# Kernel tuning notes

Measured on AMD Instinct MI355X. Metric: run time of the kernel, lower is better.

The kernel has to match this reference:

```python
import jax, jax.numpy as jnp
import numpy as np
from jax import lax

N, GH, GE, LH, LL = 19, 64, 64, 64, 2
B, T = 256, 256


def _normalized_adjacency(A):
    # A: (..., n, n). Add self-loops, symmetric degree normalization.
    n = A.shape[-1]
    A = A + jnp.eye(n, dtype=A.dtype)
    deg = jnp.clip(A.sum(axis=-1), 1e-6, None)  # (..., n)
    dis = deg ** -0.5
    return A * dis[..., :, None] * dis[..., None, :]


def _graph_encoder(A, w1_w, w1_b, w2_w, w2_b):
    # A: (B, T, n, n) -> (B, T, GE). Node features X = A rows.
    An = _normalized_adjacency(A)
    X = jax.nn.relu(An @ (A @ w1_w.T + w1_b))   # (B,T,n,GH)
    X = jax.nn.relu(An @ (X @ w2_w.T + w2_b))   # (B,T,n,GE)
    return X.mean(axis=-2)


def _lstm_layer(x, Wih, Whh, bih, bhh):
    # x: (B, T, D); PyTorch gate order i,f,g,o. Returns (B, T, H).
    Bb = x.shape[0]
    H = Whh.shape[1]
    xg = x @ Wih.T + (bih + bhh)  # precompute input contributions (B,T,4H)

    def step(carry, xt):
        h, c = carry
        gates = xt + h @ Whh.T
        i, f, g, o = jnp.split(gates, 4, axis=-1)
        c = jax.nn.sigmoid(f) * c + jax.nn.sigmoid(i) * jnp.tanh(g)
        h = jax.nn.sigmoid(o) * jnp.tanh(c)
        return (h, c), h

    h0 = jnp.zeros((Bb, H), x.dtype)
    (_, _), hs = lax.scan(step, (h0, h0), jnp.swapaxes(xg, 0, 1))
    return jnp.swapaxes(hs, 0, 1)


def setup_inputs() -> dict:
    key = jax.random.key(0)
    ks = jax.random.split(key, 20)
    s = 0.1
    inp = {
        'conn': jax.random.uniform(ks[0], (B, T, N, N), jnp.float32),
        'mask': jnp.ones((B, T), jnp.int32),
        'w1_w': jax.random.normal(ks[1], (GH, N), jnp.float32) * s,
        'w1_b': jax.random.normal(ks[2], (GH,), jnp.float32) * s,
        'w2_w': jax.random.normal(ks[3], (GE, GH), jnp.float32) * s,
        'w2_b': jax.random.normal(ks[4], (GE,), jnp.float32) * s,
        'lstm_Wih0': jax.random.normal(ks[5], (4 * LH, GE), jnp.float32) * s,
        'lstm_Whh0': jax.random.normal(ks[6], (4 * LH, LH), jnp.float32) * s,
        'lstm_bih0': jax.random.normal(ks[7], (4 * LH,), jnp.float32) * s,
        'lstm_bhh0': jax.random.normal(ks[8], (4 * LH,), jnp.float32) * s,
        'lstm_Wih1': jax.random.normal(ks[9], (4 * LH, LH), jnp.float32) * s,
        'lstm_Whh1': jax.random.normal(ks[10], (4 * LH, LH), jnp.float32) * s,
        'lstm_bih1': jax.random.normal(ks[11], (4 * LH,), jnp.float32) * s,
        'lstm_bhh1': jax.random.normal(ks[12], (4 * LH,), jnp.float32) * s,
        'fc1_w': jax.random.normal(ks[13], (32, LH), jnp.float32) * s,
        'fc1_b': jax.random.normal(ks[14], (32,), jnp.float32) * s,
        'fc2_w': jax.random.normal(ks[15], (2, 32), jnp.float32) * s,
        'fc2_b': jax.random.normal(ks[16], (2,), jnp.float32) * s,
    }
    return inp


def reference(conn, mask, w1_w, w1_b, w2_w, w2_b,
              lstm_Wih0, lstm_Whh0, lstm_bih0, lstm_bhh0,
              lstm_Wih1, lstm_Whh1, lstm_bih1, lstm_bhh1,
              fc1_w, fc1_b, fc2_w, fc2_b):
    emb = _graph_encoder(conn, w1_w, w1_b, w2_w, w2_b)  # (B,T,GE)
    mf = mask.astype(emb.dtype)
    emb = emb * mf[:, :, None]
    out = _lstm_layer(emb, lstm_Wih0, lstm_Whh0, lstm_bih0, lstm_bhh0)
    out = _lstm_layer(out, lstm_Wih1, lstm_Whh1, lstm_bih1, lstm_bhh1)  # (B,T,LH)
    lengths = jnp.clip(mask.sum(axis=1), 1, None)
    last_idx = jnp.clip(lengths - 1, 0, None)  # (B,)
    last_h = jnp.take_along_axis(out, last_idx[:, None, None], axis=1)[:, 0, :]
    h = jax.nn.relu(last_h @ fc1_w.T + fc1_b)
    return h @ fc2_w.T + fc2_b  # (B,2) logits
```

## Files before the change

### kernel.cpp

```cpp
#include <hip/hip_runtime.h>
#include <hip/hip_bf16.h>
#include <math.h>

#define GN 19
#define BB 256
#define TT 256

typedef short short8 __attribute__((ext_vector_type(8)));
typedef float f4 __attribute__((ext_vector_type(4)));

union Frag { int i[4]; short8 s; };

#define LWAIT() __asm__ volatile("s_waitcnt lgkmcnt(0)" ::: "memory")
#define WGBAR() __asm__ volatile("s_waitcnt lgkmcnt(0)\ns_barrier" ::: "memory")
#define PIN8(x) __asm__ volatile("" : "+v"(x))
#define PINF(x) __asm__ volatile("" : "+v"(x))

#define MFMA(a,b,c) __builtin_amdgcn_mfma_f32_16x16x32_bf16(a,b,c,0,0,0)

__device__ __forceinline__ int pkbf(float a, float b) {
    __hip_bfloat162 h2 = __float22bfloat162_rn(make_float2(a, b));
    union { __hip_bfloat162 h; int i; } u; u.h = h2; return u.i;
}

__device__ __forceinline__ float fexp2(float x) { return __builtin_amdgcn_exp2f(x); }
__device__ __forceinline__ float frcp(float x)  { return __builtin_amdgcn_rcpf(x); }
__device__ __forceinline__ float sigm(float x)  { return frcp(1.f + fexp2(-1.4426950408889634f * x)); }
__device__ __forceinline__ float tanha(float x) { float e = fexp2(2.8853900817779268f * x); return 1.f - 2.f * frcp(e + 1.f); }

__global__ __launch_bounds__(64) void encoder_mfma(
    const float* __restrict__ conn,
    const int*   __restrict__ mask,
    const float* __restrict__ w1_w,
    const float* __restrict__ w1_b,
    const float* __restrict__ w2_w,
    const float* __restrict__ w2_b,
    float* __restrict__ emb,
    int num_graphs)
{
    __shared__ float S[2304];
    __shared__ float dis[32];
    __shared__ float ps[256];

    const int t = threadIdx.x;
    const int l15 = t & 15;
    const int quad = t >> 4;

    float km[8];
    #pragma unroll
    for (int j = 0; j < 8; ++j) km[j] = (quad * 8 + j < GN) ? 1.f : 0.f;

    int rr[6], cc[6];
    #pragma unroll
    for (int i = 0; i < 6; ++i) {
        int e = t + 64 * i;
        rr[i] = e / GN;
        cc[i] = e - rr[i] * GN;
    }

    Frag w1F[4];
    #pragma unroll
    for (int nt = 0; nt < 4; ++nt) {
        int n = nt * 16 + l15;
        #pragma unroll
        for (int p = 0; p < 4; ++p) {
            int k0 = quad * 8 + 2 * p, k1 = k0 + 1;
            float a = (k0 < GN) ? w1_w[n * GN + k0] : 0.f;
            float b = (k1 < GN) ? w1_w[n * GN + k1] : 0.f;
            w1F[nt].i[p] = pkbf(a, b);
        }
    }
    Frag w2F[2][4];
    #pragma unroll
    for (int kt = 0; kt < 2; ++kt)
        #pragma unroll
        for (int nt = 0; nt < 4; ++nt) {
            int n = nt * 16 + l15;
            #pragma unroll
            for (int p = 0; p < 4; ++p) {
                int k = kt * 32 + quad * 8 + 2 * p;
                w2F[kt][nt].i[p] = pkbf(w2_w[n * 64 + k], w2_w[n * 64 + k + 1]);
            }
        }
    float b1v[4], b2v[4];
    #pragma unroll
    for (int nt = 0; nt < 4; ++nt) {
        b1v[nt] = w1_b[nt * 16 + l15];
        b2v[nt] = w2_b[nt * 16 + l15];
    }

    float pf[6];
    {
        int g0 = blockIdx.x < num_graphs ? blockIdx.x : 0;
        const float* Ag = conn + (size_t)g0 * (GN * GN);
        #pragma unroll
        for (int i = 0; i < 6; ++i) {
            int e = t + 64 * i;
            if (e < GN * GN) pf[i] = Ag[e];
        }
    }

    #pragma unroll 1
    for (int g = blockIdx.x; g < num_graphs; g += gridDim.x) {
        #pragma unroll
        for (int i = 0; i < 4; ++i) {
            int s = t + 64 * i;
            int row = s >> 3, c4 = s & 7;
            f4 z = {0.f, 0.f, 0.f, 0.f};
            *(f4*)&S[row * 68 + c4 * 4] = z;
        }
        LWAIT();
        #pragma unroll
        for (int i = 0; i < 6; ++i) {
            if (t + 64 * i < GN * GN) S[rr[i] * 68 + cc[i]] = pf[i];
        }
        {
            int gn = g + gridDim.x;
            const float* Ag = conn + (size_t)(gn < num_graphs ? gn : g) * (GN * GN);
            #pragma unroll
            for (int i = 0; i < 6; ++i) {
                int e = t + 64 * i;
                if (e < GN * GN) pf[i] = Ag[e];
            }
        }
        LWAIT();

        if (t < 32) {
            float dv = 0.f;
            if (t < GN) {
                float d = 1.0f;
                #pragma unroll
                for (int c4 = 0; c4 < 8; ++c4) {
                    f4 v = *(f4*)&S[t * 68 + c4 * 4];
                    d += v.x + v.y + v.z + v.w;
                }
                dv = rsqrtf(d);
            }
            dis[t] = dv;
        }
        LWAIT();

        float dk[8];
        {
            f4 v0 = *(f4*)&dis[quad * 8];
            f4 v1 = *(f4*)&dis[quad * 8 + 4];
            dk[0]=v0.x; dk[1]=v0.y; dk[2]=v0.z; dk[3]=v0.w;
            dk[4]=v1.x; dk[5]=v1.y; dk[6]=v1.z; dk[7]=v1.w;
        }
        Frag aF[2], anF[2];
        #pragma unroll
        for (int mt = 0; mt < 2; ++mt) {
            int m = l15 + 16 * mt;
            float dm = dis[m];
            f4 v0 = *(f4*)&S[m * 68 + quad * 8];
            f4 v1 = *(f4*)&S[m * 68 + quad * 8 + 4];
            float av[8] = {v0.x, v0.y, v0.z, v0.w, v1.x, v1.y, v1.z, v1.w};
            float an[8];
            #pragma unroll
            for (int j = 0; j < 8; ++j) {
                int k = quad * 8 + j;
                an[j] = (av[j] + (m == k ? 1.f : 0.f)) * dm * dk[j];
            }
            #pragma unroll
            for (int p = 0; p < 4; ++p) {
                aF[mt].i[p]  = pkbf(av[2*p], av[2*p+1]);
                anF[mt].i[p] = pkbf(an[2*p], an[2*p+1]);
            }
        }
        LWAIT();

        #pragma unroll
        for (int mt = 0; mt < 2; ++mt)
            #pragma unroll
            for (int nt = 0; nt < 4; ++nt) {
                float bb = b1v[nt];
                f4 c = {bb, bb, bb, bb};
                c = MFMA(aF[mt].s, w1F[nt].s, c);
                int col = nt * 16 + l15;
                #pragma unroll
                for (int r = 0; r < 4; ++r)
                    S[col * 36 + (mt * 16 + quad * 4 + r)] = c[r];
            }
        LWAIT();

        Frag hF[4];
        #pragma unroll
        for (int nt = 0; nt < 4; ++nt) {
            int n = nt * 16 + l15;
            f4 v0 = *(f4*)&S[n * 36 + quad * 8];
            f4 v1 = *(f4*)&S[n * 36 + quad * 8 + 4];
            float vv[8] = {v0.x, v0.y, v0.z, v0.w, v1.x, v1.y, v1.z, v1.w};
            #pragma unroll
            for (int p = 0; p < 4; ++p)
                hF[nt].i[p] = pkbf(vv[2*p] * km[2*p], vv[2*p+1] * km[2*p+1]);
        }
        LWAIT();

        #pragma unroll
        for (int mt = 0; mt < 2; ++mt)
            #pragma unroll
            for (int nt = 0; nt < 4; ++nt) {
                f4 c = {0.f, 0.f, 0.f, 0.f};
                c = MFMA(anF[mt].s, hF[nt].s, c);
                int col = nt * 16 + l15;
                #pragma unroll
                for (int r = 0; r < 4; ++r)
                    S[(mt * 16 + quad * 4 + r) * 68 + col] = fmaxf(c[r], 0.f);
            }
        LWAIT();

        Frag xF[2][2];
        #pragma unroll
        for (int mt = 0; mt < 2; ++mt) {
            int m = l15 + 16 * mt;
            #pragma unroll
            for (int kt = 0; kt < 2; ++kt) {
                f4 v0 = *(f4*)&S[m * 68 + kt * 32 + quad * 8];
                f4 v1 = *(f4*)&S[m * 68 + kt * 32 + quad * 8 + 4];
                xF[mt][kt].i[0] = pkbf(v0.x, v0.y);
                xF[mt][kt].i[1] = pkbf(v0.z, v0.w);
                xF[mt][kt].i[2] = pkbf(v1.x, v1.y);
                xF[mt][kt].i[3] = pkbf(v1.z, v1.w);
            }
        }
        LWAIT();

        #pragma unroll
        for (int mt = 0; mt < 2; ++mt)
            #pragma unroll
            for (int nt = 0; nt < 4; ++nt) {
                float bb = b2v[nt];
                f4 c = {bb, bb, bb, bb};
                c = MFMA(xF[mt][0].s, w2F[0][nt].s, c);
                c = MFMA(xF[mt][1].s, w2F[1][nt].s, c);
                int col = nt * 16 + l15;
                #pragma unroll
                for (int r = 0; r < 4; ++r)
                    S[col * 36 + (mt * 16 + quad * 4 + r)] = c[r];
            }
        LWAIT();

        Frag hG[4];
        #pragma unroll
        for (int nt = 0; nt < 4; ++nt) {
            int n = nt * 16 + l15;
            f4 v0 = *(f4*)&S[n * 36 + quad * 8];
            f4 v1 = *(f4*)&S[n * 36 + quad * 8 + 4];
            float vv[8] = {v0.x, v0.y, v0.z, v0.w, v1.x, v1.y, v1.z, v1.w};
            #pragma unroll
            for (int p = 0; p < 4; ++p)
                hG[nt].i[p] = pkbf(vv[2*p] * km[2*p], vv[2*p+1] * km[2*p+1]);
        }

        float cs[4];
        #pragma unroll
        for (int nt = 0; nt < 4; ++nt) cs[nt] = 0.f;
        #pragma unroll
        for (int mt = 0; mt < 2; ++mt)
            #pragma unroll
            for (int nt = 0; nt < 4; ++nt) {
                f4 c = {0.f, 0.f, 0.f, 0.f};
                c = MFMA(anF[mt].s, hG[nt].s, c);
                if (mt == 0) {
                    cs[nt] += fmaxf(c[0], 0.f) + fmaxf(c[1], 0.f)
                            + fmaxf(c[2], 0.f) + fmaxf(c[3], 0.f);
                } else if (quad == 0) {
                    cs[nt] += fmaxf(c[0], 0.f) + fmaxf(c[1], 0.f) + fmaxf(c[2], 0.f);
                }
            }
        #pragma unroll
        for (int nt = 0; nt < 4; ++nt)
            ps[quad * 64 + nt * 16 + l15] = cs[nt];
        LWAIT();
        float tot = ps[t] + ps[64 + t] + ps[128 + t] + ps[192 + t];
        float mf = (float)mask[g];
        emb[(size_t)g * 64 + t] = tot * (1.f / 19.f) * mf;
        LWAIT();
    }
}

__device__ __forceinline__ void unpack_h(const int* __restrict__ src,
                                         int l15, int quad,
                                         Frag* __restrict__ BHh,
                                         Frag* __restrict__ BHl)
{
    #pragma unroll
    for (int kt = 0; kt < 2; ++kt) {
        const int4* pp = (const int4*)&src[l15 * 68 + kt * 32 + quad * 8];
        int4 va = pp[0], vb = pp[1];
        BHh[kt].i[0] = (int)__builtin_amdgcn_perm((unsigned)va.y, (unsigned)va.x, 0x05040100u);
        BHh[kt].i[1] = (int)__builtin_amdgcn_perm((unsigned)va.w, (unsigned)va.z, 0x05040100u);
        BHh[kt].i[2] = (int)__builtin_amdgcn_perm((unsigned)vb.y, (unsigned)vb.x, 0x05040100u);
        BHh[kt].i[3] = (int)__builtin_amdgcn_perm((unsigned)vb.w, (unsigned)vb.z, 0x05040100u);
        BHl[kt].i[0] = (int)__builtin_amdgcn_perm((unsigned)va.y, (unsigned)va.x, 0x07060302u);
        BHl[kt].i[1] = (int)__builtin_amdgcn_perm((unsigned)va.w, (unsigned)va.z, 0x07060302u);
        BHl[kt].i[2] = (int)__builtin_amdgcn_perm((unsigned)vb.y, (unsigned)vb.x, 0x07060302u);
        BHl[kt].i[3] = (int)__builtin_amdgcn_perm((unsigned)vb.w, (unsigned)vb.z, 0x07060302u);
    }
}

__global__ __launch_bounds__(1024, 4) void lstm_mfma(
    const float* __restrict__ x,
    const int*   __restrict__ mask,
    const float* __restrict__ Wih0, const float* __restrict__ Whh0,
    const float* __restrict__ bih0, const float* __restrict__ bhh0,
    const float* __restrict__ Wih1, const float* __restrict__ Whh1,
    const float* __restrict__ bih1, const float* __restrict__ bhh1,
    const float* __restrict__ fc1_w, const float* __restrict__ fc1_b,
    const float* __restrict__ fc2_w, const float* __restrict__ fc2_b,
    float* __restrict__ out)
{
    __shared__ int   h0b[2][16 * 68];
    __shared__ int   h1b[2][16 * 68];
    __shared__ float hlast[16][68];
    __shared__ float red[512];
    __shared__ int   li_s[16];

    const int tid  = threadIdx.x;
    const int w    = tid >> 6;
    const int grp  = w >> 3;
    const int wl   = w & 7;
    const int lane = tid & 63;
    const int l15  = lane & 15;
    const int quad = lane >> 4;
    const int bb0  = blockIdx.x * 16;

    for (int i = tid; i < 16 * 68; i += 1024) h1b[0][i] = 0;

    if (tid < 512) {
        int b16 = tid >> 5, j = tid & 31;
        int s = 0;
        #pragma unroll
        for (int c8 = 0; c8 < 8; ++c8)
            s += mask[(bb0 + b16) * TT + j + 32 * c8];
        red[tid] = (float)s;
    }
    __syncthreads();
    if (tid < 16) {
        float s = 0.f;
        #pragma unroll
        for (int j = 0; j < 32; ++j) s += red[tid * 32 + j];
        int li = (int)s - 1;
        li_s[tid] = li < 0 ? 0 : (li > TT - 1 ? TT - 1 : li);
    }
    __syncthreads();
    const int li = li_s[l15];

    const float* __restrict__ Wx = grp ? Wih1 : Wih0;
    const float* __restrict__ Wh = grp ? Whh1 : Whh0;
    const float* __restrict__ bi = grp ? bih1 : bih0;
    const float* __restrict__ bh = grp ? bhh1 : bhh0;

    Frag Ax[2][2], Ah[2][2];
    f4 biasv[2];
    #pragma unroll
    for (int mt = 0; mt < 2; ++mt) {
        int mg = 2 * wl + mt;
        int orig = (l15 & 3) * 64 + (mg * 4 + (l15 >> 2));
        #pragma unroll
        for (int kt = 0; kt < 2; ++kt)
            #pragma unroll
            for (int p = 0; p < 4; ++p) {
                int k = kt * 32 + quad * 8 + 2 * p;
                Ax[mt][kt].i[p] = pkbf(Wx[orig * 64 + k], Wx[orig * 64 + k + 1]);
                Ah[mt][kt].i[p] = pkbf(Wh[orig * 64 + k], Wh[orig * 64 + k + 1]);
            }
        int uu = mg * 4 + quad;
        #pragma unroll
        for (int r = 0; r < 4; ++r)
            biasv[mt][r] = bi[r * 64 + uu] + bh[r * 64 + uu];
    }
    #pragma unroll
    for (int mt = 0; mt < 2; ++mt) {
        PIN8(Ax[mt][0].s); PIN8(Ax[mt][1].s);
        PIN8(Ah[mt][0].s); PIN8(Ah[mt][1].s);
        PINF(biasv[mt]);
    }

    const int u0 = (2 * wl + 0) * 4 + quad;
    const int u1 = (2 * wl + 1) * 4 + quad;

    Frag BX[2], BH0h[2], BH0l[2], BH1h[2], BH1l[2];
    #pragma unroll
    for (int kt = 0; kt < 2; ++kt)
        #pragma unroll
        for (int p = 0; p < 4; ++p) {
            BX[kt].i[p] = 0; BH0h[kt].i[p] = 0; BH0l[kt].i[p] = 0;
            BH1h[kt].i[p] = 0; BH1l[kt].i[p] = 0;
        }
    float cst[2] = {0.f, 0.f}, hlv[2] = {0.f, 0.f};

    const float* __restrict__ xb = x + (size_t)(bb0 + l15) * TT * 64;
    f4 xpre[4];
    if (grp == 0) {
        const f4* p0 = (const f4*)(xb + quad * 8);
        const f4* p1 = (const f4*)(xb + 32 + quad * 8);
        xpre[0] = p0[0]; xpre[1] = p0[1];
        xpre[2] = p1[0]; xpre[3] = p1[1];
    }

    #pragma unroll 1
    for (int it = 0; it <= TT; ++it) {
        const int cur = it & 1;
        f4 g[2];
        bool act = false;

        if (grp == 0) {
            if (it < TT) {
                act = true;
                #pragma unroll
                for (int kt = 0; kt < 2; ++kt) {
                    f4 v0 = xpre[kt * 2], v1 = xpre[kt * 2 + 1];
                    BX[kt].i[0] = pkbf(v0.x, v0.y);
                    BX[kt].i[1] = pkbf(v0.z, v0.w);
                    BX[kt].i[2] = pkbf(v1.x, v1.y);
                    BX[kt].i[3] = pkbf(v1.z, v1.w);
                }
                int tn = it + 1 < TT ? it + 1 : TT - 1;
                const f4* p0 = (const f4*)(xb + (size_t)tn * 64 + quad * 8);
                const f4* p1 = (const f4*)(xb + (size_t)tn * 64 + 32 + quad * 8);
                xpre[0] = p0[0]; xpre[1] = p0[1];
                xpre[2] = p1[0]; xpre[3] = p1[1];

                #pragma unroll
                for (int mt = 0; mt < 2; ++mt) {
                    f4 ca = biasv[mt];
                    ca = MFMA(Ax[mt][0].s, BX[0].s,   ca);
                    ca = MFMA(Ah[mt][0].s, BH0h[0].s, ca);
                    ca = MFMA(Ah[mt][0].s, BH0l[0].s, ca);
                    f4 cb = {0.f, 0.f, 0.f, 0.f};
                    cb = MFMA(Ax[mt][1].s, BX[1].s,   cb);
                    cb = MFMA(Ah[mt][1].s, BH0h[1].s, cb);
                    cb = MFMA(Ah[mt][1].s, BH0l[1].s, cb);
                    g[mt] = ca + cb;
                }
            }
        } else {
            if (it >= 1) {
                act = true;
                #pragma unroll
                for (int mt = 0; mt < 2; ++mt) {
                    f4 ca = biasv[mt];
                    ca = MFMA(Ax[mt][0].s, BH0h[0].s, ca);
                    ca = MFMA(Ax[mt][0].s, BH0l[0].s, ca);
                    ca = MFMA(Ah[mt][0].s, BH1h[0].s, ca);
                    ca = MFMA(Ah[mt][0].s, BH1l[0].s, ca);
                    f4 cb = {0.f, 0.f, 0.f, 0.f};
                    cb = MFMA(Ax[mt][1].s, BH0h[1].s, cb);
                    cb = MFMA(Ax[mt][1].s, BH0l[1].s, cb);
                    cb = MFMA(Ah[mt][1].s, BH1h[1].s, cb);
                    cb = MFMA(Ah[mt][1].s, BH1l[1].s, cb);
                    g[mt] = ca + cb;
                }
            }
        }

        if (act) {
            int* __restrict__ dst = grp ? h1b[cur] : h0b[cur];
            #pragma unroll
            for (int mt = 0; mt < 2; ++mt) {
                f4 gg = g[mt];
                float si = sigm(gg[0]), sf = sigm(gg[1]);
                float tg = tanha(gg[2]), so = sigm(gg[3]);
                float cc = fmaf(sf, cst[mt], si * tg);
                cst[mt] = cc;
                float h = so * tanha(cc);
                if (grp && it - 1 == li) hlv[mt] = h;
                unsigned hb = __float_as_uint(h);
                float hhi = __uint_as_float(hb & 0xFFFF0000u);
                float hlo = h - hhi;
                unsigned lopk = (unsigned)pkbf(hlo, hlo);
                int packed = (int)__builtin_amdgcn_perm(lopk, hb, 0x05040302u);
                dst[l15 * 68 + (mt ? u1 : u0)] = packed;
            }
        }

        WGBAR();

        if (it < TT) {
            unpack_h(h0b[cur], l15, quad, BH0h, BH0l);
            if (grp) unpack_h(h1b[cur], l15, quad, BH1h, BH1l);
        }
    }

    if (grp == 1) {
        hlast[l15][u0] = hlv[0];
        hlast[l15][u1] = hlv[1];
    }
    __syncthreads();
    if (tid < 512) {
        int b = tid >> 5, o = tid & 31;
        float acc = fc1_b[o];
        const float* fw = fc1_w + o * 64;
        #pragma unroll
        for (int j = 0; j < 64; ++j)
            acc = fmaf(hlast[b][j], fw[j], acc);
        red[b * 32 + o] = fmaxf(acc, 0.f);
    }
    __syncthreads();
    if (tid < 32) {
        int b = tid >> 1, o = tid & 1;
        float acc = fc2_b[o];
        #pragma unroll
        for (int j = 0; j < 32; ++j)
            acc = fmaf(fc2_w[o * 32 + j], red[b * 32 + j], acc);
        out[(bb0 + b) * 2 + o] = acc;
    }
}

extern "C" void kernel_launch(void* const* d_in, const int* in_sizes, int n_in,
                              void* d_out, int out_size, void* d_ws, size_t ws_size,
                              hipStream_t stream)
{
    const float* conn  = (const float*)d_in[0];
    const int*   mask  = (const int*)  d_in[1];
    const float* w1_w  = (const float*)d_in[2];
    const float* w1_b  = (const float*)d_in[3];
    const float* w2_w  = (const float*)d_in[4];
    const float* w2_b  = (const float*)d_in[5];
    const float* Wih0  = (const float*)d_in[6];
    const float* Whh0  = (const float*)d_in[7];
    const float* bih0  = (const float*)d_in[8];
    const float* bhh0  = (const float*)d_in[9];
    const float* Wih1  = (const float*)d_in[10];
    const float* Whh1  = (const float*)d_in[11];
    const float* bih1  = (const float*)d_in[12];
    const float* bhh1  = (const float*)d_in[13];
    const float* fc1_w = (const float*)d_in[14];
    const float* fc1_b = (const float*)d_in[15];
    const float* fc2_w = (const float*)d_in[16];
    const float* fc2_b = (const float*)d_in[17];

    float* out = (float*)d_out;
    float* emb = (float*)d_ws;

    const int num_graphs = BB * TT;

    encoder_mfma<<<8192, 64, 0, stream>>>(
        conn, mask, w1_w, w1_b, w2_w, w2_b, emb, num_graphs);

    lstm_mfma<<<16, 1024, 0, stream>>>(
        emb, mask, Wih0, Whh0, bih0, bhh0, Wih1, Whh1, bih1, bhh1,
        fc1_w, fc1_b, fc2_w, fc2_b, out);
}
```

Before: 603.8 us.

## Store embeddings as bf16 and split LSTM hidden state into hi/lo LDS planes

```diff
diff --git a/kernel.cpp b/kernel.cpp
--- a/kernel.cpp
+++ b/kernel.cpp
@@ -8,6 +8,7 @@
 
 typedef short short8 __attribute__((ext_vector_type(8)));
 typedef float f4 __attribute__((ext_vector_type(4)));
+typedef unsigned short u16;
 
 union Frag { int i[4]; short8 s; };
 
@@ -35,7 +36,7 @@
     const float* __restrict__ w1_b,
     const float* __restrict__ w2_w,
     const float* __restrict__ w2_b,
-    float* __restrict__ emb,
+    u16* __restrict__ emb,
     int num_graphs)
 {
     __shared__ float S[2304];
@@ -274,33 +275,29 @@
         LWAIT();
         float tot = ps[t] + ps[64 + t] + ps[128 + t] + ps[192 + t];
         float mf = (float)mask[g];
-        emb[(size_t)g * 64 + t] = tot * (1.f / 19.f) * mf;
+        float v = tot * (1.f / 19.f) * mf;
+        emb[(size_t)g * 64 + t] = (u16)(unsigned)pkbf(v, v);
         LWAIT();
     }
 }
 
-__device__ __forceinline__ void unpack_h(const int* __restrict__ src,
-                                         int l15, int quad,
-                                         Frag* __restrict__ BHh,
-                                         Frag* __restrict__ BHl)
+__device__ __forceinline__ void read_h2(const u16* __restrict__ hi,
+                                        const u16* __restrict__ lo,
+                                        int off, Frag* __restrict__ BHh,
+                                        Frag* __restrict__ BHl)
 {
     #pragma unroll
     for (int kt = 0; kt < 2; ++kt) {
-        const int4* pp = (const int4*)&src[l15 * 68 + kt * 32 + quad * 8];
-        int4 va = pp[0], vb = pp[1];
-        BHh[kt].i[0] = (int)__builtin_amdgcn_perm((unsigned)va.y, (unsigned)va.x, 0x05040100u);
-        BHh[kt].i[1] = (int)__builtin_amdgcn_perm((unsigned)va.w, (unsigned)va.z, 0x05040100u);
-        BHh[kt].i[2] = (int)__builtin_amdgcn_perm((unsigned)vb.y, (unsigned)vb.x, 0x05040100u);
-        BHh[kt].i[3] = (int)__builtin_amdgcn_perm((unsigned)vb.w, (unsigned)vb.z, 0x05040100u);
-        BHl[kt].i[0] = (int)__builtin_amdgcn_perm((unsigned)va.y, (unsigned)va.x, 0x07060302u);
-        BHl[kt].i[1] = (int)__builtin_amdgcn_perm((unsigned)va.w, (unsigned)va.z, 0x07060302u);
-        BHl[kt].i[2] = (int)__builtin_amdgcn_perm((unsigned)vb.y, (unsigned)vb.x, 0x07060302u);
-        BHl[kt].i[3] = (int)__builtin_amdgcn_perm((unsigned)vb.w, (unsigned)vb.z, 0x07060302u);
+        int4 vh = *(const int4*)&hi[off + kt * 32];
+        int4 vl = *(const int4*)&lo[off + kt * 32];
+        BHh[kt].i[0] = vh.x; BHh[kt].i[1] = vh.y; BHh[kt].i[2] = vh.z; BHh[kt].i[3] = vh.w;
+        BHl[kt].i[0] = vl.x; BHl[kt].i[1] = vl.y; BHl[kt].i[2] = vl.z; BHl[kt].i[3] = vl.w;
     }
 }
 
-__global__ __launch_bounds__(1024, 4) void lstm_mfma(
-    const float* __restrict__ x,
+__global__ __launch_bounds__(1024) __attribute__((amdgpu_waves_per_eu(4, 4)))
+void lstm_mfma(
+    const u16*   __restrict__ x,
     const int*   __restrict__ mask,
     const float* __restrict__ Wih0, const float* __restrict__ Whh0,
     const float* __restrict__ bih0, const float* __restrict__ bhh0,
@@ -310,8 +307,10 @@
     const float* __restrict__ fc2_w, const float* __restrict__ fc2_b,
     float* __restrict__ out)
 {
-    __shared__ int   h0b[2][16 * 68];
-    __shared__ int   h1b[2][16 * 68];
+    __shared__ __attribute__((aligned(16))) u16 h0hi[2][16 * 72];
+    __shared__ __attribute__((aligned(16))) u16 h0lo[2][16 * 72];
+    __shared__ __attribute__((aligned(16))) u16 h1hi[2][16 * 72];
+    __shared__ __attribute__((aligned(16))) u16 h1lo[2][16 * 72];
     __shared__ float hlast[16][68];
     __shared__ float red[512];
     __shared__ int   li_s[16];
@@ -325,7 +324,7 @@
     const int quad = lane >> 4;
     const int bb0  = blockIdx.x * 16;
 
-    for (int i = tid; i < 16 * 68; i += 1024) h1b[0][i] = 0;
+    for (int i = tid; i < 16 * 72; i += 1024) { h1hi[0][i] = 0; h1lo[0][i] = 0; }
 
     if (tid < 512) {
         int b16 = tid >> 5, j = tid & 31;
@@ -379,24 +378,22 @@
 
     const int u0 = (2 * wl + 0) * 4 + quad;
     const int u1 = (2 * wl + 1) * 4 + quad;
-
-    Frag BX[2], BH0h[2], BH0l[2], BH1h[2], BH1l[2];
+    const int hoff = l15 * 72 + quad * 8;
+
+    Frag BH0h[2], BH0l[2], BH1h[2], BH1l[2], BXn[2];
     #pragma unroll
     for (int kt = 0; kt < 2; ++kt)
         #pragma unroll
         for (int p = 0; p < 4; ++p) {
-            BX[kt].i[p] = 0; BH0h[kt].i[p] = 0; BH0l[kt].i[p] = 0;
+            BXn[kt].i[p] = 0; BH0h[kt].i[p] = 0; BH0l[kt].i[p] = 0;
             BH1h[kt].i[p] = 0; BH1l[kt].i[p] = 0;
         }
     float cst[2] = {0.f, 0.f}, hlv[2] = {0.f, 0.f};
 
-    const float* __restrict__ xb = x + (size_t)(bb0 + l15) * TT * 64;
-    f4 xpre[4];
+    const u16* __restrict__ xb = x + (size_t)(bb0 + l15) * TT * 64;
     if (grp == 0) {
-        const f4* p0 = (const f4*)(xb + quad * 8);
-        const f4* p1 = (const f4*)(xb + 32 + quad * 8);
-        xpre[0] = p0[0]; xpre[1] = p0[1];
-        xpre[2] = p1[0]; xpre[3] = p1[1];
+        BXn[0] = *(const Frag*)&xb[quad * 8];
+        BXn[1] = *(const Frag*)&xb[32 + quad * 8];
     }
 
     #pragma unroll 1
@@ -408,30 +405,21 @@
         if (grp == 0) {
             if (it < TT) {
                 act = true;
-                #pragma unroll
-                for (int kt = 0; kt < 2; ++kt) {
-                    f4 v0 = xpre[kt * 2], v1 = xpre[kt * 2 + 1];
-                    BX[kt].i[0] = pkbf(v0.x, v0.y);
-                    BX[kt].i[1] = pkbf(v0.z, v0.w);
-                    BX[kt].i[2] = pkbf(v1.x, v1.y);
-                    BX[kt].i[3] = pkbf(v1.z, v1.w);
-                }
+                Frag bx0 = BXn[0], bx1 = BXn[1];
                 int tn = it + 1 < TT ? it + 1 : TT - 1;
-                const f4* p0 = (const f4*)(xb + (size_t)tn * 64 + quad * 8);
-                const f4* p1 = (const f4*)(xb + (size_t)tn * 64 + 32 + quad * 8);
-                xpre[0] = p0[0]; xpre[1] = p0[1];
-                xpre[2] = p1[0]; xpre[3] = p1[1];
+                BXn[0] = *(const Frag*)&xb[(size_t)tn * 64 + quad * 8];
+                BXn[1] = *(const Frag*)&xb[(size_t)tn * 64 + 32 + quad * 8];
 
                 #pragma unroll
                 for (int mt = 0; mt < 2; ++mt) {
                     f4 ca = biasv[mt];
-                    ca = MFMA(Ax[mt][0].s, BX[0].s,   ca);
-                    ca = MFMA(Ah[mt][0].s, BH0h[0].s, ca);
-                    ca = MFMA(Ah[mt][0].s, BH0l[0].s, ca);
+                    ca = MFMA(Ax[mt][0].s, bx0.s,      ca);
+                    ca = MFMA(Ah[mt][0].s, BH0h[0].s,  ca);
+                    ca = MFMA(Ah[mt][0].s, BH0l[0].s,  ca);
                     f4 cb = {0.f, 0.f, 0.f, 0.f};
-                    cb = MFMA(Ax[mt][1].s, BX[1].s,   cb);
-                    cb = MFMA(Ah[mt][1].s, BH0h[1].s, cb);
-                    cb = MFMA(Ah[mt][1].s, BH0l[1].s, cb);
+                    cb = MFMA(Ax[mt][1].s, bx1.s,      cb);
+                    cb = MFMA(Ah[mt][1].s, BH0h[1].s,  cb);
+                    cb = MFMA(Ah[mt][1].s, BH0l[1].s,  cb);
                     g[mt] = ca + cb;
                 }
             }
@@ -456,7 +444,8 @@
         }
 
         if (act) {
-            int* __restrict__ dst = grp ? h1b[cur] : h0b[cur];
+            u16* __restrict__ dhi = grp ? h1hi[cur] : h0hi[cur];
+            u16* __restrict__ dlo = grp ? h1lo[cur] : h0lo[cur];
             #pragma unroll
             for (int mt = 0; mt < 2; ++mt) {
                 f4 gg = g[mt];
@@ -469,17 +458,17 @@
                 unsigned hb = __float_as_uint(h);
                 float hhi = __uint_as_float(hb & 0xFFFF0000u);
                 float hlo = h - hhi;
-                unsigned lopk = (unsigned)pkbf(hlo, hlo);
-                int packed = (int)__builtin_amdgcn_perm(lopk, hb, 0x05040302u);
-                dst[l15 * 68 + (mt ? u1 : u0)] = packed;
+                int uu = mt ? u1 : u0;
+                dhi[l15 * 72 + uu] = (u16)(hb >> 16);
+                dlo[l15 * 72 + uu] = (u16)(unsigned)pkbf(hlo, hlo);
             }
         }
 
         WGBAR();
 
         if (it < TT) {
-            unpack_h(h0b[cur], l15, quad, BH0h, BH0l);
-            if (grp) unpack_h(h1b[cur], l15, quad, BH1h, BH1l);
+            read_h2(h0hi[cur], h0lo[cur], hoff, BH0h, BH0l);
+            if (grp) read_h2(h1hi[cur], h1lo[cur], hoff, BH1h, BH1l);
         }
     }
 
@@ -532,7 +521,7 @@
     const float* fc2_b = (const float*)d_in[17];
 
     float* out = (float*)d_out;
-    float* emb = (float*)d_ws;
+    u16*   emb = (u16*)d_ws;
 
     const int num_graphs = BB * TT;
 
```

Result: faster. 589.0 us (-2.4%).
